# Performance work log

Measured on AMD Instinct MI355X. Metric: run time of the kernel, lower is better.

The kernel has to match this reference:

```python
import jax, jax.numpy as jnp
import numpy as np

N_NODES = 100000
N_EDGES = 1600000
IN_FEATS = 64
HIDDEN = 64
N_CLASSES = 1


def setup_inputs() -> dict:
    key = jax.random.key(0)
    k0, k1, k2, k3, k4 = jax.random.split(key, 5)
    x = jax.random.normal(k0, (N_NODES, IN_FEATS), dtype=jnp.float32)
    src = jax.random.randint(k1, (N_EDGES,), 0, N_NODES, dtype=jnp.int32)
    dst = jax.random.randint(k2, (N_EDGES,), 0, N_NODES, dtype=jnp.int32)
    W1 = jax.random.normal(k3, (IN_FEATS, HIDDEN), dtype=jnp.float32) * (1.0 / np.sqrt(IN_FEATS))
    b1 = jnp.zeros((HIDDEN,), dtype=jnp.float32)
    W2 = jax.random.normal(k4, (HIDDEN, N_CLASSES), dtype=jnp.float32) * (1.0 / np.sqrt(HIDDEN))
    b2 = jnp.zeros((N_CLASSES,), dtype=jnp.float32)
    return {"x": x, "src": src, "dst": dst, "W1": W1, "b1": b1, "W2": W2, "b2": b2}


def _graph_conv(h, src, dst, W, b, n_nodes):
    # DGL GraphConv, norm='both': D_out^{-1/2} A D_in^{-1/2} h W + b
    ones = jnp.ones(src.shape[0], dtype=h.dtype)
    deg_out = jax.ops.segment_sum(ones, src, num_segments=n_nodes)
    deg_in = jax.ops.segment_sum(ones, dst, num_segments=n_nodes)
    norm_out = jnp.where(deg_out > 0, deg_out, 1.0) ** -0.5  # [N]
    norm_in = jnp.where(deg_in > 0, deg_in, 1.0) ** -0.5
    h = h * norm_out[:, None]
    # project first when it shrinks the message size (matches DGL's in>out path; math identical)
    if W.shape[1] < W.shape[0]:
        h = h @ W
    agg = jax.ops.segment_sum(h[src], dst, num_segments=n_nodes)  # [N, d]
    agg = agg * norm_in[:, None]
    if W.shape[1] >= W.shape[0]:
        agg = agg @ W
    return agg + b


def reference(x, src, dst, W1, b1, W2, b2):
    h = _graph_conv(x, src, dst, W1, b1, N_NODES)
    h = jax.nn.relu(h)
    # dropout p=0.0 -> identity
    h = _graph_conv(h, src, dst, W2, b2, N_NODES)
    return jax.nn.sigmoid(h)
```

## Files before the change

### kernel.cpp

```cpp
#include <hip/hip_runtime.h>

#define NN 100000
#define NE 1600000
#define NW 25000
#define NW4 6250
#define S_D 64
#define EPS_D (NE / S_D)
#define S_S 64
#define EPS_S (NE / S_S)
#define AGG_GRID 2048
#define REPLAY_NB ((NE + 255) / 256)
#define PROJ_NB   ((NN / 16 + 3) / 4)

typedef unsigned int uint;
typedef _Float16 f16x8 __attribute__((ext_vector_type(8)));
typedef _Float16 f16x2 __attribute__((ext_vector_type(2)));
typedef float f32x4 __attribute__((ext_vector_type(4)));

__global__ void __launch_bounds__(256)
k_hist(const int* __restrict__ src, const int* __restrict__ dst,
       uint* __restrict__ partial_in, uint* __restrict__ partial_out,
       unsigned char* __restrict__ lr) {
    __shared__ uint4 cnt4[NW4];
    uint* cnt = (uint*)cnt4;
    int sl = blockIdx.x;
    int y  = blockIdx.y;
    for (int w = threadIdx.x; w < NW4; w += 256) cnt4[w] = make_uint4(0, 0, 0, 0);
    __syncthreads();
    if (y == 0) {
        int base = sl * EPS_D;
        for (int i4 = threadIdx.x; i4 < EPS_D / 4; i4 += 256) {
            int e = base + i4 * 4;
            int4 k4 = *(const int4*)&dst[e];
            uint sh0 = (uint)(k4.x & 3) * 8u, sh1 = (uint)(k4.y & 3) * 8u;
            uint sh2 = (uint)(k4.z & 3) * 8u, sh3 = (uint)(k4.w & 3) * 8u;
            uint r0 = (atomicAdd(&cnt[k4.x >> 2], 1u << sh0) >> sh0) & 0xffu;
            uint r1 = (atomicAdd(&cnt[k4.y >> 2], 1u << sh1) >> sh1) & 0xffu;
            uint r2 = (atomicAdd(&cnt[k4.z >> 2], 1u << sh2) >> sh2) & 0xffu;
            uint r3 = (atomicAdd(&cnt[k4.w >> 2], 1u << sh3) >> sh3) & 0xffu;
            uchar4 pk = make_uchar4((unsigned char)r0, (unsigned char)r1,
                                    (unsigned char)r2, (unsigned char)r3);
            *(uchar4*)&lr[e] = pk;
        }
        __syncthreads();
        uint4* dp = (uint4*)(partial_in + (size_t)sl * NW);
        for (int w = threadIdx.x; w < NW4; w += 256) dp[w] = cnt4[w];
    } else {
        int base = sl * EPS_S;
        for (int i4 = threadIdx.x; i4 < EPS_S / 4; i4 += 256) {
            int e = base + i4 * 4;
            int4 k4 = *(const int4*)&src[e];
            atomicAdd(&cnt[k4.x >> 2], 1u << ((uint)(k4.x & 3) * 8u));
            atomicAdd(&cnt[k4.y >> 2], 1u << ((uint)(k4.y & 3) * 8u));
            atomicAdd(&cnt[k4.z >> 2], 1u << ((uint)(k4.z & 3) * 8u));
            atomicAdd(&cnt[k4.w >> 2], 1u << ((uint)(k4.w & 3) * 8u));
        }
        __syncthreads();
        uint4* dp = (uint4*)(partial_out + (size_t)sl * NW);
        for (int w = threadIdx.x; w < NW4; w += 256) dp[w] = cnt4[w];
    }
}

__global__ void k_degnorm(uint* __restrict__ partial_in, const uint* __restrict__ partial_out,
                          int* __restrict__ deg_in, float* __restrict__ norm_in,
                          float* __restrict__ norm_out, int* __restrict__ bsum) {
    __shared__ int red[4];
    int w = blockIdx.x * 256 + threadIdx.x;
    int mysum = 0;
    if (w < NW) {
        uint run = 0;
#pragma unroll 8
        for (int s = 0; s < S_D; ++s) {
            uint u = partial_in[(size_t)s * NW + w];
            partial_in[(size_t)s * NW + w] = run;
            run += u;
        }
        uint ro = 0;
#pragma unroll 8
        for (int s = 0; s < S_S; ++s) ro += partial_out[(size_t)s * NW + w];
        int4 dg;
        float4 fi, fo;
        int d0 = run & 0xff, d1 = (run >> 8) & 0xff, d2 = (run >> 16) & 0xff, d3 = (run >> 24) & 0xff;
        dg = make_int4(d0, d1, d2, d3);
        fi.x = d0 > 0 ? rsqrtf((float)d0) : 1.0f;
        fi.y = d1 > 0 ? rsqrtf((float)d1) : 1.0f;
        fi.z = d2 > 0 ? rsqrtf((float)d2) : 1.0f;
        fi.w = d3 > 0 ? rsqrtf((float)d3) : 1.0f;
        int o0 = ro & 0xff, o1 = (ro >> 8) & 0xff, o2 = (ro >> 16) & 0xff, o3 = (ro >> 24) & 0xff;
        fo.x = o0 > 0 ? rsqrtf((float)o0) : 1.0f;
        fo.y = o1 > 0 ? rsqrtf((float)o1) : 1.0f;
        fo.z = o2 > 0 ? rsqrtf((float)o2) : 1.0f;
        fo.w = o3 > 0 ? rsqrtf((float)o3) : 1.0f;
        *(int4*)&deg_in[w * 4]     = dg;
        *(float4*)&norm_in[w * 4]  = fi;
        *(float4*)&norm_out[w * 4] = fo;
        mysum = d0 + d1 + d2 + d3;
    }
#pragma unroll
    for (int off = 32; off; off >>= 1) mysum += __shfl_xor(mysum, off, 64);
    if ((threadIdx.x & 63) == 0) red[threadIdx.x >> 6] = mysum;
    __syncthreads();
    if (threadIdx.x == 0) bsum[blockIdx.x] = red[0] + red[1] + red[2] + red[3];
}

__global__ void k_scan(const int* __restrict__ deg_in, const int* __restrict__ bsum,
                       int* __restrict__ row_ofs, int nb) {
    __shared__ int wofs[4];
    __shared__ int sbofs;
    int t = threadIdx.x;
    if (t < 64) {
        int lane = t;
        int v0 = (lane * 2     < nb) ? bsum[lane * 2]     : 0;
        int v1 = (lane * 2 + 1 < nb) ? bsum[lane * 2 + 1] : 0;
        int pair = v0 + v1;
        int pre = pair;
#pragma unroll
        for (int off = 1; off < 64; off <<= 1) {
            int u = __shfl_up(pre, off, 64);
            if (lane >= off) pre += u;
        }
        int basep = pre - pair;
        int bx = blockIdx.x;
        int b   = __shfl(basep, bx >> 1, 64);
        int v0b = __shfl(v0,    bx >> 1, 64);
        if (lane == 0) sbofs = (bx & 1) ? b + v0b : b;
        if (blockIdx.x == 0 && lane == 63) row_ofs[NN] = pre;
    }
    int base = blockIdx.x * 1024 + t * 4;
    int d[4];
#pragma unroll
    for (int k = 0; k < 4; ++k) {
        int n = base + k;
        d[k] = (n < NN) ? deg_in[n] : 0;
    }
    int loc = d[0] + d[1] + d[2] + d[3];
    int v = loc;
    int lane = t & 63;
#pragma unroll
    for (int off = 1; off < 64; off <<= 1) {
        int u = __shfl_up(v, off, 64);
        if (lane >= off) v += u;
    }
    if (lane == 63) wofs[t >> 6] = v;
    __syncthreads();
    int w = t >> 6;
    int wbase = 0;
    if (w > 0) wbase += wofs[0];
    if (w > 1) wbase += wofs[1];
    if (w > 2) wbase += wofs[2];
    int excl = sbofs + wbase + (v - loc);
#pragma unroll
    for (int k = 0; k < 4; ++k) {
        int n = base + k;
        if (n < NN) { row_ofs[n] = excl; excl += d[k]; }
    }
}

__global__ void __launch_bounds__(256)
k_repl_proj(const int* __restrict__ src, const int* __restrict__ dst,
            const uint* __restrict__ base_bytes, const unsigned char* __restrict__ lr,
            const int* __restrict__ row_ofs, int* __restrict__ csr_src,
            const float* __restrict__ x, const float* __restrict__ norm_out,
            const float* __restrict__ W1, _Float16* __restrict__ y) {
    if (blockIdx.x < REPLAY_NB) {
        int e = blockIdx.x * 256 + threadIdx.x;
        if (e < NE) {
            int d  = dst[e];
            int sl = e / EPS_D;
            uint pw = base_bytes[(size_t)sl * NW + (d >> 2)];
            int b = (int)((pw >> ((d & 3) * 8)) & 0xffu);
            csr_src[row_ofs[d] + b + (int)lr[e]] = src[e];
        }
        return;
    }
    int lane = threadIdx.x & 63;
    int col  = lane & 15;
    int kh   = lane >> 4;
    f16x8 wf[4][2];
#pragma unroll
    for (int t = 0; t < 4; ++t)
#pragma unroll
        for (int s = 0; s < 2; ++s)
#pragma unroll
            for (int j = 0; j < 8; ++j)
                wf[t][s][j] = (_Float16)W1[(s * 32 + kh * 8 + j) * 64 + t * 16 + col];
    int tile = (blockIdx.x - REPLAY_NB) * 4 + (threadIdx.x >> 6);
    if (tile >= NN / 16) return;
    int base = tile * 16;
    int row  = base + col;
    float no = norm_out[row];
    const float* xr = &x[(size_t)row * 64 + kh * 8];
    f16x8 af[2];
#pragma unroll
    for (int s = 0; s < 2; ++s) {
        float4 v0 = *(const float4*)&xr[s * 32];
        float4 v1 = *(const float4*)&xr[s * 32 + 4];
        af[s][0] = (_Float16)(v0.x * no); af[s][1] = (_Float16)(v0.y * no);
        af[s][2] = (_Float16)(v0.z * no); af[s][3] = (_Float16)(v0.w * no);
        af[s][4] = (_Float16)(v1.x * no); af[s][5] = (_Float16)(v1.y * no);
        af[s][6] = (_Float16)(v1.z * no); af[s][7] = (_Float16)(v1.w * no);
    }
    f32x4 acc[4];
#pragma unroll
    for (int t = 0; t < 4; ++t) acc[t] = (f32x4){0.f, 0.f, 0.f, 0.f};
#pragma unroll
    for (int t = 0; t < 4; ++t) {
        acc[t] = __builtin_amdgcn_mfma_f32_16x16x32_f16(af[0], wf[t][0], acc[t], 0, 0, 0);
        acc[t] = __builtin_amdgcn_mfma_f32_16x16x32_f16(af[1], wf[t][1], acc[t], 0, 0, 0);
    }
#pragma unroll
    for (int t = 0; t < 4; ++t)
#pragma unroll
        for (int r = 0; r < 4; ++r)
            y[(size_t)(base + kh * 4 + r) * 64 + t * 16 + col] = (_Float16)acc[t][r];
}

__device__ inline float2 up2(uint u) {
    f16x2 p = __builtin_bit_cast(f16x2, u);
    return make_float2((float)p.x, (float)p.y);
}

__global__ void __launch_bounds__(256)
k_agg1(const int* __restrict__ csr_src, const int* __restrict__ row_ofs,
       const uint* __restrict__ xb, const float* __restrict__ norm_in,
       const float* __restrict__ norm_out,
       const float* __restrict__ b1, const float* __restrict__ W2,
       float* __restrict__ z) {
    int tid = threadIdx.x;
    int lane = tid & 63, q = lane >> 4, lq = lane & 15;
    float4 bb = *(const float4*)&b1[lq * 4];
    float4 ww = *(const float4*)&W2[lq * 4];
    const size_t lqo = (size_t)(lq << 3);
    for (int n = blockIdx.x * 4 + (tid >> 6); n < NN; n += AGG_GRID * 4) {
        int beg = row_ofs[n], end = row_ofs[n + 1];
        float a0 = 0, a1 = 0, a2 = 0, a3 = 0;
        int ei = beg + q;
        for (; ei + 12 < end; ei += 16) {
            int s0 = csr_src[ei], s1 = csr_src[ei + 4];
            int s2 = csr_src[ei + 8], s3 = csr_src[ei + 12];
            uint2 u0 = *(const uint2*)((const char*)xb + ((size_t)s0 << 7) + lqo);
            uint2 u1 = *(const uint2*)((const char*)xb + ((size_t)s1 << 7) + lqo);
            uint2 u2 = *(const uint2*)((const char*)xb + ((size_t)s2 << 7) + lqo);
            uint2 u3 = *(const uint2*)((const char*)xb + ((size_t)s3 << 7) + lqo);
            float2 p0 = up2(u0.x), r0 = up2(u0.y);
            float2 p1 = up2(u1.x), r1 = up2(u1.y);
            float2 p2 = up2(u2.x), r2 = up2(u2.y);
            float2 p3 = up2(u3.x), r3 = up2(u3.y);
            a0 += (p0.x + p1.x) + (p2.x + p3.x);
            a1 += (p0.y + p1.y) + (p2.y + p3.y);
            a2 += (r0.x + r1.x) + (r2.x + r3.x);
            a3 += (r0.y + r1.y) + (r2.y + r3.y);
        }
        for (; ei < end; ei += 4) {
            int s0 = csr_src[ei];
            uint2 u0 = *(const uint2*)((const char*)xb + ((size_t)s0 << 7) + lqo);
            float2 p0 = up2(u0.x), r0 = up2(u0.y);
            a0 += p0.x; a1 += p0.y; a2 += r0.x; a3 += r0.y;
        }
        a0 += __shfl_xor(a0, 16, 64); a0 += __shfl_xor(a0, 32, 64);
        a1 += __shfl_xor(a1, 16, 64); a1 += __shfl_xor(a1, 32, 64);
        a2 += __shfl_xor(a2, 16, 64); a2 += __shfl_xor(a2, 32, 64);
        a3 += __shfl_xor(a3, 16, 64); a3 += __shfl_xor(a3, 32, 64);
        float nin = norm_in[n];
        float h0 = fmaxf(a0 * nin + bb.x, 0.0f);
        float h1 = fmaxf(a1 * nin + bb.y, 0.0f);
        float h2 = fmaxf(a2 * nin + bb.z, 0.0f);
        float h3 = fmaxf(a3 * nin + bb.w, 0.0f);
        float zv = h0 * ww.x + h1 * ww.y + h2 * ww.z + h3 * ww.w;
#pragma unroll
        for (int off = 8; off; off >>= 1) zv += __shfl_xor(zv, off, 64);
        if (lane == 0) z[n] = zv * norm_out[n];
    }
}

__global__ void k_out2(const int* __restrict__ csr_src, const int* __restrict__ row_ofs,
                       const float* __restrict__ z, const float* __restrict__ norm_in,
                       const float* __restrict__ b2, float* __restrict__ out) {
    int n = blockIdx.x * blockDim.x + threadIdx.x;
    if (n < NN) {
        int beg = row_ofs[n], end = row_ofs[n + 1];
        float a = 0.0f;
        int i = beg;
        for (; i + 3 < end; i += 4) {
            float z0 = z[csr_src[i]], z1 = z[csr_src[i + 1]];
            float z2 = z[csr_src[i + 2]], z3 = z[csr_src[i + 3]];
            a += (z0 + z1) + (z2 + z3);
        }
        for (; i < end; ++i) a += z[csr_src[i]];
        float v = a * norm_in[n] + b2[0];
        out[n] = 1.0f / (1.0f + expf(-v));
    }
}


extern "C" void kernel_launch(void* const* d_in, const int* in_sizes, int n_in,
                              void* d_out, int out_size, void* d_ws, size_t ws_size,
                              hipStream_t stream) {
    const float* x   = (const float*)d_in[0];
    const int*   src = (const int*)d_in[1];
    const int*   dst = (const int*)d_in[2];
    const float* W1  = (const float*)d_in[3];
    const float* b1  = (const float*)d_in[4];
    const float* W2  = (const float*)d_in[5];
    const float* b2  = (const float*)d_in[6];
    float* out = (float*)d_out;

    uint* W0 = (uint*)d_ws;
    unsigned char* lr          = (unsigned char*)W0;
    uint*          partial_in  = W0 + 400000;
    int*           csr_src     = (int*)(W0 + 2000000);
    uint*          partial_out = W0 + 3600000;
    uint*          xb          = W0 + 3600000;
    int*           row_ofs     = (int*)(W0 + 6800000);
    int*           deg_in      = row_ofs + NN + 32;
    float*         norm_in     = (float*)(deg_in + NN);
    float*         norm_out    = norm_in + NN;
    float*         z           = norm_out + NN;
    int*           bsum        = (int*)(z + NN);

    int nb = (NN + 1023) / 1024;

    k_hist     <<<dim3(S_D, 2), 256, 0, stream>>>(src, dst, partial_in, partial_out, lr);
    k_degnorm  <<<nb, 256, 0, stream>>>(partial_in, partial_out, deg_in, norm_in,
                                        norm_out, bsum);
    k_scan     <<<nb, 256, 0, stream>>>(deg_in, bsum, row_ofs, nb);
    k_repl_proj<<<REPLAY_NB + PROJ_NB, 256, 0, stream>>>(src, dst, partial_in, lr,
                                                         row_ofs, csr_src, x, norm_out,
                                                         W1, (_Float16*)xb);
    k_agg1     <<<AGG_GRID, 256, 0, stream>>>(csr_src, row_ofs, xb, norm_in, norm_out,
                                              b1, W2, z);
    k_out2     <<<(NN + 255) / 256, 256, 0, stream>>>(csr_src, row_ofs, z, norm_in, b2, out);
}
```

Measured before the change: 126.5 us.

## Split histogram node range in half and fuse degree-norm with decoupled-lookback scan

The histogram kernel now splits the node-word range across two blocks per edge slice. This halves the LDS histogram so more blocks fit per CU and doubles the grid, at the cost of each block reading every edge and skipping half of them. The separate degree/norm and scan kernels are merged into one kernel that publishes per-block totals through a flag array with acquire/release spin-waits. That removes one launch and the deg_in round trip, but adds a memset and relies on earlier blocks being scheduled before later ones.

```diff
diff --git a/kernel.cpp b/kernel.cpp
--- a/kernel.cpp
+++ b/kernel.cpp
@@ -3,11 +3,11 @@
 #define NN 100000
 #define NE 1600000
 #define NW 25000
-#define NW4 6250
+#define NWH 12500
+#define NWH4 3125
 #define S_D 64
-#define EPS_D (NE / S_D)
 #define S_S 64
-#define EPS_S (NE / S_S)
+#define EPS (NE / S_D)
 #define AGG_GRID 2048
 #define REPLAY_NB ((NE + 255) / 256)
 #define PROJ_NB   ((NN / 16 + 3) / 4)
@@ -21,52 +21,90 @@
 k_hist(const int* __restrict__ src, const int* __restrict__ dst,
        uint* __restrict__ partial_in, uint* __restrict__ partial_out,
        unsigned char* __restrict__ lr) {
-    __shared__ uint4 cnt4[NW4];
+    __shared__ uint4 cnt4[NWH4];
     uint* cnt = (uint*)cnt4;
     int sl = blockIdx.x;
-    int y  = blockIdx.y;
-    for (int w = threadIdx.x; w < NW4; w += 256) cnt4[w] = make_uint4(0, 0, 0, 0);
+    int is_src = blockIdx.y >> 1;
+    uint wbase = (blockIdx.y & 1) * NWH;
+    for (int w = threadIdx.x; w < NWH4; w += 256) cnt4[w] = make_uint4(0, 0, 0, 0);
     __syncthreads();
-    if (y == 0) {
-        int base = sl * EPS_D;
-        for (int i4 = threadIdx.x; i4 < EPS_D / 4; i4 += 256) {
+    int base = sl * EPS;
+    if (!is_src) {
+        for (int i4 = threadIdx.x; i4 < EPS / 4; i4 += 256) {
             int e = base + i4 * 4;
             int4 k4 = *(const int4*)&dst[e];
-            uint sh0 = (uint)(k4.x & 3) * 8u, sh1 = (uint)(k4.y & 3) * 8u;
-            uint sh2 = (uint)(k4.z & 3) * 8u, sh3 = (uint)(k4.w & 3) * 8u;
-            uint r0 = (atomicAdd(&cnt[k4.x >> 2], 1u << sh0) >> sh0) & 0xffu;
-            uint r1 = (atomicAdd(&cnt[k4.y >> 2], 1u << sh1) >> sh1) & 0xffu;
-            uint r2 = (atomicAdd(&cnt[k4.z >> 2], 1u << sh2) >> sh2) & 0xffu;
-            uint r3 = (atomicAdd(&cnt[k4.w >> 2], 1u << sh3) >> sh3) & 0xffu;
-            uchar4 pk = make_uchar4((unsigned char)r0, (unsigned char)r1,
-                                    (unsigned char)r2, (unsigned char)r3);
-            *(uchar4*)&lr[e] = pk;
+            {
+                uint rw = (uint)(k4.x >> 2) - wbase;
+                if (rw < NWH) {
+                    uint sh = (uint)(k4.x & 3) * 8u;
+                    uint old = atomicAdd(&cnt[rw], 1u << sh);
+                    lr[e] = (unsigned char)((old >> sh) & 0xffu);
+                }
+            }
+            {
+                uint rw = (uint)(k4.y >> 2) - wbase;
+                if (rw < NWH) {
+                    uint sh = (uint)(k4.y & 3) * 8u;
+                    uint old = atomicAdd(&cnt[rw], 1u << sh);
+                    lr[e + 1] = (unsigned char)((old >> sh) & 0xffu);
+                }
+            }
+            {
+                uint rw = (uint)(k4.z >> 2) - wbase;
+                if (rw < NWH) {
+                    uint sh = (uint)(k4.z & 3) * 8u;
+                    uint old = atomicAdd(&cnt[rw], 1u << sh);
+                    lr[e + 2] = (unsigned char)((old >> sh) & 0xffu);
+                }
+            }
+            {
+                uint rw = (uint)(k4.w >> 2) - wbase;
+                if (rw < NWH) {
+                    uint sh = (uint)(k4.w & 3) * 8u;
+                    uint old = atomicAdd(&cnt[rw], 1u << sh);
+                    lr[e + 3] = (unsigned char)((old >> sh) & 0xffu);
+                }
+            }
         }
         __syncthreads();
-        uint4* dp = (uint4*)(partial_in + (size_t)sl * NW);
-        for (int w = threadIdx.x; w < NW4; w += 256) dp[w] = cnt4[w];
+        uint4* dp = (uint4*)(partial_in + (size_t)sl * NW + wbase);
+        for (int w = threadIdx.x; w < NWH4; w += 256) dp[w] = cnt4[w];
     } else {
-        int base = sl * EPS_S;
-        for (int i4 = threadIdx.x; i4 < EPS_S / 4; i4 += 256) {
+        for (int i4 = threadIdx.x; i4 < EPS / 4; i4 += 256) {
             int e = base + i4 * 4;
             int4 k4 = *(const int4*)&src[e];
-            atomicAdd(&cnt[k4.x >> 2], 1u << ((uint)(k4.x & 3) * 8u));
-            atomicAdd(&cnt[k4.y >> 2], 1u << ((uint)(k4.y & 3) * 8u));
-            atomicAdd(&cnt[k4.z >> 2], 1u << ((uint)(k4.z & 3) * 8u));
-            atomicAdd(&cnt[k4.w >> 2], 1u << ((uint)(k4.w & 3) * 8u));
+            {
+                uint rw = (uint)(k4.x >> 2) - wbase;
+                if (rw < NWH) atomicAdd(&cnt[rw], 1u << ((uint)(k4.x & 3) * 8u));
+            }
+            {
+                uint rw = (uint)(k4.y >> 2) - wbase;
+                if (rw < NWH) atomicAdd(&cnt[rw], 1u << ((uint)(k4.y & 3) * 8u));
+            }
+            {
+                uint rw = (uint)(k4.z >> 2) - wbase;
+                if (rw < NWH) atomicAdd(&cnt[rw], 1u << ((uint)(k4.z & 3) * 8u));
+            }
+            {
+                uint rw = (uint)(k4.w >> 2) - wbase;
+                if (rw < NWH) atomicAdd(&cnt[rw], 1u << ((uint)(k4.w & 3) * 8u));
+            }
         }
         __syncthreads();
-        uint4* dp = (uint4*)(partial_out + (size_t)sl * NW);
-        for (int w = threadIdx.x; w < NW4; w += 256) dp[w] = cnt4[w];
-    }
-}
-
-__global__ void k_degnorm(uint* __restrict__ partial_in, const uint* __restrict__ partial_out,
-                          int* __restrict__ deg_in, float* __restrict__ norm_in,
-                          float* __restrict__ norm_out, int* __restrict__ bsum) {
+        uint4* dp = (uint4*)(partial_out + (size_t)sl * NW + wbase);
+        for (int w = threadIdx.x; w < NWH4; w += 256) dp[w] = cnt4[w];
+    }
+}
+
+__global__ void __launch_bounds__(256)
+k_degscan(uint* __restrict__ partial_in, const uint* __restrict__ partial_out,
+          float* __restrict__ norm_in, float* __restrict__ norm_out,
+          int* __restrict__ row_ofs, int* __restrict__ look, int nb) {
     __shared__ int red[4];
-    int w = blockIdx.x * 256 + threadIdx.x;
-    int mysum = 0;
+    __shared__ int s_excl;
+    int t = threadIdx.x;
+    int w = blockIdx.x * 256 + t;
+    int d0 = 0, d1 = 0, d2 = 0, d3 = 0;
     if (w < NW) {
         uint run = 0;
 #pragma unroll 8
@@ -78,10 +116,8 @@
         uint ro = 0;
 #pragma unroll 8
         for (int s = 0; s < S_S; ++s) ro += partial_out[(size_t)s * NW + w];
-        int4 dg;
+        d0 = run & 0xff; d1 = (run >> 8) & 0xff; d2 = (run >> 16) & 0xff; d3 = (run >> 24) & 0xff;
         float4 fi, fo;
-        int d0 = run & 0xff, d1 = (run >> 8) & 0xff, d2 = (run >> 16) & 0xff, d3 = (run >> 24) & 0xff;
-        dg = make_int4(d0, d1, d2, d3);
         fi.x = d0 > 0 ? rsqrtf((float)d0) : 1.0f;
         fi.y = d1 > 0 ? rsqrtf((float)d1) : 1.0f;
         fi.z = d2 > 0 ? rsqrtf((float)d2) : 1.0f;
@@ -91,49 +127,10 @@
         fo.y = o1 > 0 ? rsqrtf((float)o1) : 1.0f;
         fo.z = o2 > 0 ? rsqrtf((float)o2) : 1.0f;
         fo.w = o3 > 0 ? rsqrtf((float)o3) : 1.0f;
-        *(int4*)&deg_in[w * 4]     = dg;
         *(float4*)&norm_in[w * 4]  = fi;
         *(float4*)&norm_out[w * 4] = fo;
-        mysum = d0 + d1 + d2 + d3;
-    }
-#pragma unroll
-    for (int off = 32; off; off >>= 1) mysum += __shfl_xor(mysum, off, 64);
-    if ((threadIdx.x & 63) == 0) red[threadIdx.x >> 6] = mysum;
-    __syncthreads();
-    if (threadIdx.x == 0) bsum[blockIdx.x] = red[0] + red[1] + red[2] + red[3];
-}
-
-__global__ void k_scan(const int* __restrict__ deg_in, const int* __restrict__ bsum,
-                       int* __restrict__ row_ofs, int nb) {
-    __shared__ int wofs[4];
-    __shared__ int sbofs;
-    int t = threadIdx.x;
-    if (t < 64) {
-        int lane = t;
-        int v0 = (lane * 2     < nb) ? bsum[lane * 2]     : 0;
-        int v1 = (lane * 2 + 1 < nb) ? bsum[lane * 2 + 1] : 0;
-        int pair = v0 + v1;
-        int pre = pair;
-#pragma unroll
-        for (int off = 1; off < 64; off <<= 1) {
-            int u = __shfl_up(pre, off, 64);
-            if (lane >= off) pre += u;
-        }
-        int basep = pre - pair;
-        int bx = blockIdx.x;
-        int b   = __shfl(basep, bx >> 1, 64);
-        int v0b = __shfl(v0,    bx >> 1, 64);
-        if (lane == 0) sbofs = (bx & 1) ? b + v0b : b;
-        if (blockIdx.x == 0 && lane == 63) row_ofs[NN] = pre;
-    }
-    int base = blockIdx.x * 1024 + t * 4;
-    int d[4];
-#pragma unroll
-    for (int k = 0; k < 4; ++k) {
-        int n = base + k;
-        d[k] = (n < NN) ? deg_in[n] : 0;
-    }
-    int loc = d[0] + d[1] + d[2] + d[3];
+    }
+    int loc = d0 + d1 + d2 + d3;
     int v = loc;
     int lane = t & 63;
 #pragma unroll
@@ -141,19 +138,42 @@
         int u = __shfl_up(v, off, 64);
         if (lane >= off) v += u;
     }
-    if (lane == 63) wofs[t >> 6] = v;
+    if (lane == 63) red[t >> 6] = v;
     __syncthreads();
-    int w = t >> 6;
-    int wbase = 0;
-    if (w > 0) wbase += wofs[0];
-    if (w > 1) wbase += wofs[1];
-    if (w > 2) wbase += wofs[2];
-    int excl = sbofs + wbase + (v - loc);
-#pragma unroll
-    for (int k = 0; k < 4; ++k) {
-        int n = base + k;
-        if (n < NN) { row_ofs[n] = excl; excl += d[k]; }
-    }
+    if (t < 64) {
+        if (t == 0) {
+            int total = red[0] + red[1] + red[2] + red[3];
+            __hip_atomic_store(&look[blockIdx.x], total + 1,
+                               __ATOMIC_RELEASE, __HIP_MEMORY_SCOPE_AGENT);
+        }
+        int sum = 0;
+        for (int i = t; i < blockIdx.x; i += 64) {
+            int vv;
+            do {
+                vv = __hip_atomic_load(&look[i], __ATOMIC_ACQUIRE, __HIP_MEMORY_SCOPE_AGENT);
+            } while (vv == 0);
+            sum += vv - 1;
+        }
+#pragma unroll
+        for (int off = 32; off; off >>= 1) sum += __shfl_xor(sum, off, 64);
+        if (t == 0) s_excl = sum;
+    }
+    __syncthreads();
+    int wv = t >> 6;
+    int wbase2 = 0;
+    if (wv > 0) wbase2 += red[0];
+    if (wv > 1) wbase2 += red[1];
+    if (wv > 2) wbase2 += red[2];
+    int excl = s_excl + wbase2 + (v - loc);
+    if (w < NW) {
+        int n = w * 4;
+        row_ofs[n] = excl;     excl += d0;
+        row_ofs[n + 1] = excl; excl += d1;
+        row_ofs[n + 2] = excl; excl += d2;
+        row_ofs[n + 3] = excl;
+    }
+    if (blockIdx.x == nb - 1 && t == 0)
+        row_ofs[NN] = s_excl + red[0] + red[1] + red[2] + red[3];
 }
 
 __global__ void __launch_bounds__(256)
@@ -166,7 +186,7 @@
         int e = blockIdx.x * 256 + threadIdx.x;
         if (e < NE) {
             int d  = dst[e];
-            int sl = e / EPS_D;
+            int sl = e / EPS;
             uint pw = base_bytes[(size_t)sl * NW + (d >> 2)];
             int b = (int)((pw >> ((d & 3) * 8)) & 0xffu);
             csr_src[row_ofs[d] + b + (int)lr[e]] = src[e];
@@ -312,18 +332,17 @@
     uint*          partial_out = W0 + 3600000;
     uint*          xb          = W0 + 3600000;
     int*           row_ofs     = (int*)(W0 + 6800000);
-    int*           deg_in      = row_ofs + NN + 32;
-    float*         norm_in     = (float*)(deg_in + NN);
+    float*         norm_in     = (float*)(row_ofs + NN + 32);
     float*         norm_out    = norm_in + NN;
     float*         z           = norm_out + NN;
-    int*           bsum        = (int*)(z + NN);
+    int*           look        = (int*)(z + NN);
 
     int nb = (NN + 1023) / 1024;
 
-    k_hist     <<<dim3(S_D, 2), 256, 0, stream>>>(src, dst, partial_in, partial_out, lr);
-    k_degnorm  <<<nb, 256, 0, stream>>>(partial_in, partial_out, deg_in, norm_in,
-                                        norm_out, bsum);
-    k_scan     <<<nb, 256, 0, stream>>>(deg_in, bsum, row_ofs, nb);
+    hipMemsetAsync(look, 0, 512, stream);
+    k_hist     <<<dim3(S_D, 4), 256, 0, stream>>>(src, dst, partial_in, partial_out, lr);
+    k_degscan  <<<nb, 256, 0, stream>>>(partial_in, partial_out, norm_in, norm_out,
+                                        row_ofs, look, nb);
     k_repl_proj<<<REPLAY_NB + PROJ_NB, 256, 0, stream>>>(src, dst, partial_in, lr,
                                                          row_ofs, csr_src, x, norm_out,
                                                          W1, (_Float16*)xb);
```

Measured after the change: 135.3 us. 7.0% more time.
